# Kernel optimization log

Measured on AMD Instinct MI355X. Metric: run time of the kernel, lower is better.

## Reference

```python
import jax, jax.numpy as jnp
import numpy as np

N_NODES = 100000
N_EDGES = 1600000


def setup_inputs() -> dict:
    key = jax.random.key(0)
    k1, k2, k3, k4 = jax.random.split(key, 4)
    in_c, hid_c, out_c = 128, 128, 64
    x = jax.random.normal(k1, (N_NODES, in_c), dtype=jnp.float32)
    edge_index = jax.random.randint(k2, (2, N_EDGES), 0, N_NODES, dtype=jnp.int64)
    W1 = jax.random.normal(k3, (in_c, hid_c), dtype=jnp.float32) * (1.0 / np.sqrt(in_c))
    b1 = jnp.zeros((hid_c,), dtype=jnp.float32)
    W2 = jax.random.normal(k4, (hid_c, out_c), dtype=jnp.float32) * (1.0 / np.sqrt(hid_c))
    b2 = jnp.zeros((out_c,), dtype=jnp.float32)
    return {"x": x, "edge_index": edge_index, "W1": W1, "b1": b1, "W2": W2, "b2": b2}


def reference(x, edge_index, W1, b1, W2, b2):
    # PyG GCNConv default: add self-loops, symmetric deg normalization, bias.
    N = x.shape[0]
    loops = jnp.arange(N, dtype=edge_index.dtype)
    src = jnp.concatenate([edge_index[0], loops])  # message sources (j)
    dst = jnp.concatenate([edge_index[1], loops])  # aggregation targets (i)
    ones = jnp.ones(src.shape[0], dtype=x.dtype)
    deg = jax.ops.segment_sum(ones, dst, num_segments=N)  # in-degree incl. self-loops
    dis = jnp.where(deg > 0, jax.lax.rsqrt(deg), 0.0)     # deg^{-1/2}, inf->0
    norm = dis[src] * dis[dst]                             # [E+N]

    def gcn(h, W, b):
        h = h @ W                                  # linear transform first (fewer bytes moved)
        msg = h[src] * norm[:, None]               # gather + scale, [E+N, C]
        return jax.ops.segment_sum(msg, dst, num_segments=N) + b

    h = jax.nn.relu(gcn(x, W1, b1))
    return gcn(h, W2, b2)
```

## Files before the change

### kernel.cpp

```cpp
#include <hip/hip_runtime.h>


constexpr int NBKT = 512;
constexpr int EPB  = 4096;
constexpr int CAP  = 8192;

using short8 = __attribute__((ext_vector_type(8))) short;
using f32x4  = __attribute__((ext_vector_type(4))) float;

__device__ __forceinline__ unsigned short f2bf(float f) {
  unsigned u = __float_as_uint(f);
  unsigned r = (u + 0x7FFFu + ((u >> 16) & 1u)) >> 16;
  return (unsigned short)r;
}
__device__ __forceinline__ float bf2f(unsigned short h) {
  return __uint_as_float(((unsigned)h) << 16);
}

__device__ __forceinline__ int ld_idx(const void* ei, int is64, long long i) {
  return is64 ? (int)((const long long*)ei)[i] : ((const int*)ei)[i];
}

__device__ __forceinline__ int sniff64(const unsigned* ei, int tid) {
  unsigned v = (tid < 128) ? ei[2 * tid + 1] : 0u;
  return __syncthreads_or((int)(v != 0u)) ? 0 : 1;
}

__global__ __launch_bounds__(256) void k_partition(const void* __restrict__ ei,
                                                   int* __restrict__ bkt_cursor,
                                                   unsigned* __restrict__ pairbuf,
                                                   int e, int npb) {
  __shared__ int hcnt[NBKT];
  int blk = blockIdx.x, tid = threadIdx.x;
  int is64 = sniff64((const unsigned*)ei, tid);
  for (int i = tid; i < NBKT; i += 256) hcnt[i] = 0;
  __syncthreads();
  int base = blk * EPB;
  int end = base + EPB; if (end > e) end = e;
  for (int i = base + tid; i < end; i += 256) {
    int d = ld_idx(ei, is64, (long long)e + i);
    atomicAdd(&hcnt[d / npb], 1);
  }
  __syncthreads();
  for (int i = tid; i < NBKT; i += 256) {
    int c = hcnt[i];
    hcnt[i] = c ? (i * CAP + atomicAdd(&bkt_cursor[i * 16], c)) : 0;
  }
  __syncthreads();
  for (int i = base + tid; i < end; i += 256) {
    int s = ld_idx(ei, is64, i);
    int d = ld_idx(ei, is64, (long long)e + i);
    int bkt = d / npb;
    int pos = atomicAdd(&hcnt[bkt], 1);
    pairbuf[pos] = (unsigned)s | ((unsigned)(d - bkt * npb) << 20);
  }
}

__global__ __launch_bounds__(256) void k_bucket_all(const unsigned* __restrict__ pairbuf,
                                                    const int* __restrict__ bkt_cursor,
                                                    int2* __restrict__ rowse,
                                                    int* __restrict__ cursor,
                                                    float* __restrict__ dis,
                                                    int* __restrict__ csr,
                                                    int n, int npb) {
  __shared__ int lcsr[CAP];
  __shared__ int cnt[256];
  __shared__ int scn[256];
  int b = blockIdx.x, tid = threadIdx.x;
  int lo = b * npb;
  if (lo >= n) return;
  int hi = lo + npb; if (hi > n) hi = n;
  int nn = hi - lo;
  int seg_base = b * CAP;
  int cnt_total = bkt_cursor[b * 16];

  for (int i = tid; i < nn; i += 256) cnt[i] = 0;
  __syncthreads();
  for (int i = tid; i < cnt_total; i += 256)
    atomicAdd(&cnt[pairbuf[seg_base + i] >> 20], 1);
  __syncthreads();

  int v = (tid < nn) ? cnt[tid] : 0;
  scn[tid] = v;
  __syncthreads();
  for (int off = 1; off < 256; off <<= 1) {
    int t = (tid >= off) ? scn[tid - off] : 0;
    __syncthreads();
    scn[tid] += t;
    __syncthreads();
  }
  int start = (tid == 0) ? 0 : scn[tid - 1];
  if (tid < nn) {
    int node = lo + tid;
    int lo_e = seg_base + start;
    rowse[node] = make_int2(lo_e, lo_e + v);
    cursor[node] = lo_e;
    dis[node] = rsqrtf((float)(v + 1));
  }
  __syncthreads();
  if (tid < nn) cnt[tid] = start;
  __syncthreads();

  if (cnt_total <= CAP) {
    for (int i = tid; i < cnt_total; i += 256) {
      unsigned p = pairbuf[seg_base + i];
      int q = atomicAdd(&cnt[p >> 20], 1);
      lcsr[q] = (int)(p & 0xFFFFFu);
    }
    __syncthreads();
    for (int i = tid; i < cnt_total; i += 256) csr[seg_base + i] = lcsr[i];
  } else {
    for (int i = tid; i < cnt_total; i += 256) {
      unsigned p = pairbuf[seg_base + i];
      int q = atomicAdd(&cursor[lo + (int)(p >> 20)], 1);
      csr[q] = (int)(p & 0xFFFFFu);
    }
  }
}

template <int NCOL, bool XBF16>
__global__ __launch_bounds__(256) void k_gemm_mfma(const void* __restrict__ Xv,
                                                   const float* __restrict__ W,
                                                   const float* __restrict__ dis,
                                                   unsigned short* __restrict__ S,
                                                   int nrows) {
  constexpr int ROWS = 64;
  constexpr int NCF = NCOL / 16;
  __shared__ __align__(16) unsigned short xs[ROWS * 128];
  __shared__ __align__(16) unsigned short wt[NCOL * 128];
  int tid = threadIdx.x;

  for (int id = tid; id < 128 * NCOL; id += 256) {
    int k = id / NCOL, c = id % NCOL;
    wt[(c * 128 + k) ^ ((c & 7) << 3)] = f2bf(W[id]);
  }

  int wv = tid >> 6, lane = tid & 63;
  int l16 = lane & 15, lk = lane >> 4;
  int arow = wv * 16 + l16;
  int npass = (nrows + ROWS - 1) / ROWS;

  for (int p = blockIdx.x; p < npass; p += gridDim.x) {
    int r0 = p * ROWS;
    __syncthreads();
#pragma unroll
    for (int it = 0; it < 4; ++it) {
      int id = tid + 256 * it;
      int row = id >> 4, kc = id & 15;
      int gr = r0 + row;
      unsigned short v[8];
      if (gr < nrows) {
        if (XBF16) {
          const unsigned short* xb = (const unsigned short*)Xv + (size_t)gr * 128 + kc * 8;
#pragma unroll
          for (int j = 0; j < 8; ++j) v[j] = xb[j];
        } else {
          const float4* x4 = (const float4*)Xv + (size_t)gr * 32 + kc * 2;
          float4 f0 = x4[0], f1 = x4[1];
          v[0] = f2bf(f0.x); v[1] = f2bf(f0.y); v[2] = f2bf(f0.z); v[3] = f2bf(f0.w);
          v[4] = f2bf(f1.x); v[5] = f2bf(f1.y); v[6] = f2bf(f1.z); v[7] = f2bf(f1.w);
        }
      } else {
#pragma unroll
        for (int j = 0; j < 8; ++j) v[j] = 0;
      }
      int idx = (row * 128 + kc * 8) ^ ((row & 7) << 3);
      *(short8*)&xs[idx] = *(short8*)v;
    }
    __syncthreads();

    short8 a[4];
#pragma unroll
    for (int ks = 0; ks < 4; ++ks)
      a[ks] = *(short8*)&xs[(arow * 128 + ks * 32 + lk * 8) ^ ((arow & 7) << 3)];

    f32x4 acc[NCF];
#pragma unroll
    for (int cf = 0; cf < NCF; ++cf) acc[cf] = (f32x4){0.f, 0.f, 0.f, 0.f};

#pragma unroll
    for (int cf = 0; cf < NCF; ++cf) {
      int col = cf * 16 + l16;
#pragma unroll
      for (int ks = 0; ks < 4; ++ks) {
        short8 bfr = *(short8*)&wt[(col * 128 + ks * 32 + lk * 8) ^ ((col & 7) << 3)];
        acc[cf] = __builtin_amdgcn_mfma_f32_16x16x32_bf16(a[ks], bfr, acc[cf], 0, 0, 0);
      }
    }

#pragma unroll
    for (int r = 0; r < 4; ++r) {
      int gr = r0 + wv * 16 + lk * 4 + r;
      if (gr < nrows) {
        float dv = dis[gr];
#pragma unroll
        for (int cf = 0; cf < NCF; ++cf)
          S[(size_t)gr * NCOL + cf * 16 + l16] = f2bf(acc[cf][r] * dv);
      }
    }
  }
}

__global__ __launch_bounds__(256) void k_agg1(const unsigned short* __restrict__ S,
                                              const int2* __restrict__ rowse,
                                              const int* __restrict__ csr,
                                              const float* __restrict__ dis,
                                              const float* __restrict__ b1,
                                              unsigned short* __restrict__ H, int n) {
  int node = blockIdx.x * 4 + (threadIdx.x >> 6);
  if (node >= n) return;
  int lane = threadIdx.x & 63;
  int eg = lane >> 4;
  int cp = lane & 15;
  float acc[8];
  if (eg == 0) {
    short8 v = *(const short8*)&S[(size_t)node * 128 + cp * 8];
#pragma unroll
    for (int k = 0; k < 8; ++k) acc[k] = bf2f((unsigned short)v[k]);
  } else {
#pragma unroll
    for (int k = 0; k < 8; ++k) acc[k] = 0.f;
  }
  int2 rp = rowse[node];
  int e = rp.x + eg;
  for (; e + 4 < rp.y; e += 8) {
    int j0 = csr[e], j1 = csr[e + 4];
    short8 v0 = *(const short8*)&S[(size_t)j0 * 128 + cp * 8];
    short8 v1 = *(const short8*)&S[(size_t)j1 * 128 + cp * 8];
#pragma unroll
    for (int k = 0; k < 8; ++k)
      acc[k] += bf2f((unsigned short)v0[k]) + bf2f((unsigned short)v1[k]);
  }
  if (e < rp.y) {
    int j = csr[e];
    short8 v = *(const short8*)&S[(size_t)j * 128 + cp * 8];
#pragma unroll
    for (int k = 0; k < 8; ++k) acc[k] += bf2f((unsigned short)v[k]);
  }
#pragma unroll
  for (int k = 0; k < 8; ++k) {
    acc[k] += __shfl_xor(acc[k], 16);
    acc[k] += __shfl_xor(acc[k], 32);
  }
  if (eg == 0) {
    float d = dis[node];
    float4 bb0 = ((const float4*)b1)[cp * 2];
    float4 bb1 = ((const float4*)b1)[cp * 2 + 1];
    float bv[8] = {bb0.x, bb0.y, bb0.z, bb0.w, bb1.x, bb1.y, bb1.z, bb1.w};
    short8 o;
#pragma unroll
    for (int k = 0; k < 8; ++k)
      o[k] = (short)f2bf(fmaxf(fmaf(acc[k], d, bv[k]), 0.f));
    *(short8*)&H[(size_t)node * 128 + cp * 8] = o;
  }
}

__global__ __launch_bounds__(256) void k_agg2(const unsigned short* __restrict__ S,
                                              const int2* __restrict__ rowse,
                                              const int* __restrict__ csr,
                                              const float* __restrict__ dis,
                                              const float* __restrict__ b2,
                                              float* __restrict__ O, int n) {
  int node = blockIdx.x * 4 + (threadIdx.x >> 6);
  if (node >= n) return;
  int lane = threadIdx.x & 63;
  int eg = lane >> 3;
  int cp = lane & 7;
  float acc[8];
  if (eg == 0) {
    short8 v = *(const short8*)&S[(size_t)node * 64 + cp * 8];
#pragma unroll
    for (int k = 0; k < 8; ++k) acc[k] = bf2f((unsigned short)v[k]);
  } else {
#pragma unroll
    for (int k = 0; k < 8; ++k) acc[k] = 0.f;
  }
  int2 rp = rowse[node];
  int e = rp.x + eg;
  for (; e + 8 < rp.y; e += 16) {
    int j0 = csr[e], j1 = csr[e + 8];
    short8 v0 = *(const short8*)&S[(size_t)j0 * 64 + cp * 8];
    short8 v1 = *(const short8*)&S[(size_t)j1 * 64 + cp * 8];
#pragma unroll
    for (int k = 0; k < 8; ++k)
      acc[k] += bf2f((unsigned short)v0[k]) + bf2f((unsigned short)v1[k]);
  }
  if (e < rp.y) {
    int j = csr[e];
    short8 v = *(const short8*)&S[(size_t)j * 64 + cp * 8];
#pragma unroll
    for (int k = 0; k < 8; ++k) acc[k] += bf2f((unsigned short)v[k]);
  }
#pragma unroll
  for (int k = 0; k < 8; ++k) {
    acc[k] += __shfl_xor(acc[k], 8);
    acc[k] += __shfl_xor(acc[k], 16);
    acc[k] += __shfl_xor(acc[k], 32);
  }
  if (eg == 0) {
    float d = dis[node];
    float4 bb0 = ((const float4*)b2)[cp * 2];
    float4 bb1 = ((const float4*)b2)[cp * 2 + 1];
    float bv[8] = {bb0.x, bb0.y, bb0.z, bb0.w, bb1.x, bb1.y, bb1.z, bb1.w};
    float4 o0, o1;
    o0.x = fmaf(acc[0], d, bv[0]); o0.y = fmaf(acc[1], d, bv[1]);
    o0.z = fmaf(acc[2], d, bv[2]); o0.w = fmaf(acc[3], d, bv[3]);
    o1.x = fmaf(acc[4], d, bv[4]); o1.y = fmaf(acc[5], d, bv[5]);
    o1.z = fmaf(acc[6], d, bv[6]); o1.w = fmaf(acc[7], d, bv[7]);
    ((float4*)O)[(size_t)node * 16 + cp * 2] = o0;
    ((float4*)O)[(size_t)node * 16 + cp * 2 + 1] = o1;
  }
}

extern "C" void kernel_launch(void* const* d_in, const int* in_sizes, int n_in,
                              void* d_out, int out_size, void* d_ws, size_t ws_size,
                              hipStream_t stream) {
  const float* x  = (const float*)d_in[0];
  const void*  ei = d_in[1];
  const float* W1 = (const float*)d_in[2];
  const float* b1 = (const float*)d_in[3];
  const float* W2 = (const float*)d_in[4];
  const float* b2 = (const float*)d_in[5];
  float* out = (float*)d_out;

  const int N = in_sizes[0] / 128;
  const int E = in_sizes[1] / 2;
  const int npb  = (N + NBKT - 1) / NBKT;
  const int nblk = (E + EPB - 1) / EPB;

  char* w = (char*)d_ws;
  size_t off = 0;
  auto alloc = [&](size_t bytes) -> void* {
    void* p = (void*)(w + off);
    off += (bytes + 255) & ~(size_t)255;
    return p;
  };
  int2*           rowse      = (int2*)alloc((size_t)N * 8);
  int*            cursor     = (int*)alloc((size_t)N * 4);
  float*          dis        = (float*)alloc((size_t)N * 4);
  int*            csr        = (int*)alloc((size_t)NBKT * CAP * 4);
  unsigned*       pairbuf    = (unsigned*)alloc((size_t)NBKT * CAP * 4);
  unsigned short* s1         = (unsigned short*)alloc((size_t)N * 128 * 2);
  unsigned short* s2         = (unsigned short*)alloc((size_t)N * 64 * 2);
  unsigned short* h          = (unsigned short*)alloc((size_t)N * 128 * 2);
  int*            bkt_cursor = (int*)alloc((size_t)NBKT * 64);

  hipMemsetAsync(bkt_cursor, 0, (size_t)NBKT * 64, stream);
  k_partition<<<nblk, 256, 0, stream>>>(ei, bkt_cursor, pairbuf, E, npb);
  k_bucket_all<<<NBKT, 256, 0, stream>>>(pairbuf, bkt_cursor, rowse, cursor, dis,
                                         csr, N, npb);

  k_gemm_mfma<128, false><<<1024, 256, 0, stream>>>(x, W1, dis, s1, N);
  k_agg1<<<(N + 3) / 4, 256, 0, stream>>>(s1, rowse, csr, dis, b1, h, N);
  k_gemm_mfma<64, true><<<1024, 256, 0, stream>>>(h, W2, dis, s2, N);
  k_agg2<<<(N + 3) / 4, 256, 0, stream>>>(s2, rowse, csr, dis, b2, out, N);
}
```

Baseline: 200.1 us.

## Fuse first-layer aggregation with second-layer GEMM via MFMA in LDS

Replaces the separate k_agg1 kernel and the second k_gemm_mfma launch with a single kernel, k_agg1_mm. Each 512-thread block aggregates 8 nodes into a bf16 hidden tile in LDS, then runs a 16x16x32 MFMA against W2 to write the scaled s2 rows directly. This removes the global write and re-read of the hidden activation buffer h and one kernel launch. In exchange, every block reloads W2 from global memory and converts it to bf16 in LDS. Half of each MFMA tile is idle because only 8 of its 16 rows hold real nodes.

```diff
diff --git a/kernel.cpp b/kernel.cpp
--- a/kernel.cpp
+++ b/kernel.cpp
@@ -201,57 +201,92 @@
   }
 }
 
-__global__ __launch_bounds__(256) void k_agg1(const unsigned short* __restrict__ S,
-                                              const int2* __restrict__ rowse,
-                                              const int* __restrict__ csr,
-                                              const float* __restrict__ dis,
-                                              const float* __restrict__ b1,
-                                              unsigned short* __restrict__ H, int n) {
-  int node = blockIdx.x * 4 + (threadIdx.x >> 6);
-  if (node >= n) return;
-  int lane = threadIdx.x & 63;
+__global__ __launch_bounds__(512) void k_agg1_mm(const unsigned short* __restrict__ S,
+                                                 const int2* __restrict__ rowse,
+                                                 const int* __restrict__ csr,
+                                                 const float* __restrict__ dis,
+                                                 const float* __restrict__ b1,
+                                                 const float* __restrict__ W2,
+                                                 unsigned short* __restrict__ S2,
+                                                 int n) {
+  __shared__ __align__(16) unsigned short wt2[64 * 128];
+  __shared__ __align__(16) unsigned short hs[16 * 128];
+  int tid = threadIdx.x;
+  for (int id = tid; id < 64 * 128; id += 512) {
+    int k = id >> 6, c = id & 63;
+    wt2[(c * 128 + k) ^ ((c & 7) << 3)] = f2bf(W2[id]);
+  }
+
+  int wv = tid >> 6, lane = tid & 63;
+  int node = blockIdx.x * 8 + wv;
   int eg = lane >> 4;
   int cp = lane & 15;
-  float acc[8];
-  if (eg == 0) {
-    short8 v = *(const short8*)&S[(size_t)node * 128 + cp * 8];
-#pragma unroll
-    for (int k = 0; k < 8; ++k) acc[k] = bf2f((unsigned short)v[k]);
-  } else {
-#pragma unroll
-    for (int k = 0; k < 8; ++k) acc[k] = 0.f;
-  }
-  int2 rp = rowse[node];
-  int e = rp.x + eg;
-  for (; e + 4 < rp.y; e += 8) {
-    int j0 = csr[e], j1 = csr[e + 4];
-    short8 v0 = *(const short8*)&S[(size_t)j0 * 128 + cp * 8];
-    short8 v1 = *(const short8*)&S[(size_t)j1 * 128 + cp * 8];
-#pragma unroll
-    for (int k = 0; k < 8; ++k)
-      acc[k] += bf2f((unsigned short)v0[k]) + bf2f((unsigned short)v1[k]);
-  }
-  if (e < rp.y) {
-    int j = csr[e];
-    short8 v = *(const short8*)&S[(size_t)j * 128 + cp * 8];
-#pragma unroll
-    for (int k = 0; k < 8; ++k) acc[k] += bf2f((unsigned short)v[k]);
-  }
-#pragma unroll
-  for (int k = 0; k < 8; ++k) {
-    acc[k] += __shfl_xor(acc[k], 16);
-    acc[k] += __shfl_xor(acc[k], 32);
-  }
-  if (eg == 0) {
-    float d = dis[node];
-    float4 bb0 = ((const float4*)b1)[cp * 2];
-    float4 bb1 = ((const float4*)b1)[cp * 2 + 1];
-    float bv[8] = {bb0.x, bb0.y, bb0.z, bb0.w, bb1.x, bb1.y, bb1.z, bb1.w};
-    short8 o;
-#pragma unroll
-    for (int k = 0; k < 8; ++k)
-      o[k] = (short)f2bf(fmaxf(fmaf(acc[k], d, bv[k]), 0.f));
-    *(short8*)&H[(size_t)node * 128 + cp * 8] = o;
+
+  if (node < n) {
+    float acc[8];
+    if (eg == 0) {
+      short8 v = *(const short8*)&S[(size_t)node * 128 + cp * 8];
+#pragma unroll
+      for (int k = 0; k < 8; ++k) acc[k] = bf2f((unsigned short)v[k]);
+    } else {
+#pragma unroll
+      for (int k = 0; k < 8; ++k) acc[k] = 0.f;
+    }
+    int2 rp = rowse[node];
+    int e = rp.x + eg;
+    for (; e + 4 < rp.y; e += 8) {
+      int j0 = csr[e], j1 = csr[e + 4];
+      short8 v0 = *(const short8*)&S[(size_t)j0 * 128 + cp * 8];
+      short8 v1 = *(const short8*)&S[(size_t)j1 * 128 + cp * 8];
+#pragma unroll
+      for (int k = 0; k < 8; ++k)
+        acc[k] += bf2f((unsigned short)v0[k]) + bf2f((unsigned short)v1[k]);
+    }
+    if (e < rp.y) {
+      int j = csr[e];
+      short8 v = *(const short8*)&S[(size_t)j * 128 + cp * 8];
+#pragma unroll
+      for (int k = 0; k < 8; ++k) acc[k] += bf2f((unsigned short)v[k]);
+    }
+#pragma unroll
+    for (int k = 0; k < 8; ++k) {
+      acc[k] += __shfl_xor(acc[k], 16);
+      acc[k] += __shfl_xor(acc[k], 32);
+    }
+    if (eg == 0) {
+      float d = dis[node];
+      float4 bb0 = ((const float4*)b1)[cp * 2];
+      float4 bb1 = ((const float4*)b1)[cp * 2 + 1];
+      float bv[8] = {bb0.x, bb0.y, bb0.z, bb0.w, bb1.x, bb1.y, bb1.z, bb1.w};
+      short8 o;
+#pragma unroll
+      for (int k = 0; k < 8; ++k)
+        o[k] = (short)f2bf(fmaxf(fmaf(acc[k], d, bv[k]), 0.f));
+      *(short8*)&hs[(wv * 128 + cp * 8) ^ ((wv & 7) << 3)] = o;
+    }
+  }
+  __syncthreads();
+
+  if (wv < 4) {
+    int l16 = lane & 15, lk = lane >> 4;
+    short8 a[4];
+#pragma unroll
+    for (int ks = 0; ks < 4; ++ks)
+      a[ks] = *(short8*)&hs[(l16 * 128 + ks * 32 + lk * 8) ^ ((l16 & 7) << 3)];
+    f32x4 c_ = (f32x4){0.f, 0.f, 0.f, 0.f};
+    int col = wv * 16 + l16;
+#pragma unroll
+    for (int ks = 0; ks < 4; ++ks) {
+      short8 bfr = *(short8*)&wt2[(col * 128 + ks * 32 + lk * 8) ^ ((col & 7) << 3)];
+      c_ = __builtin_amdgcn_mfma_f32_16x16x32_bf16(a[ks], bfr, c_, 0, 0, 0);
+    }
+#pragma unroll
+    for (int r = 0; r < 4; ++r) {
+      int row = lk * 4 + r;
+      int gr = blockIdx.x * 8 + row;
+      if (row < 8 && gr < n)
+        S2[(size_t)gr * 64 + wv * 16 + l16] = f2bf(c_[r] * dis[gr]);
+    }
   }
 }
 
@@ -342,7 +377,6 @@
   unsigned*       pairbuf    = (unsigned*)alloc((size_t)NBKT * CAP * 4);
   unsigned short* s1         = (unsigned short*)alloc((size_t)N * 128 * 2);
   unsigned short* s2         = (unsigned short*)alloc((size_t)N * 64 * 2);
-  unsigned short* h          = (unsigned short*)alloc((size_t)N * 128 * 2);
   int*            bkt_cursor = (int*)alloc((size_t)NBKT * 64);
 
   hipMemsetAsync(bkt_cursor, 0, (size_t)NBKT * 64, stream);
@@ -351,7 +385,6 @@
                                          csr, N, npb);
 
   k_gemm_mfma<128, false><<<1024, 256, 0, stream>>>(x, W1, dis, s1, N);
-  k_agg1<<<(N + 3) / 4, 256, 0, stream>>>(s1, rowse, csr, dis, b1, h, N);
-  k_gemm_mfma<64, true><<<1024, 256, 0, stream>>>(h, W2, dis, s2, N);
+  k_agg1_mm<<<(N + 7) / 8, 512, 0, stream>>>(s1, rowse, csr, dis, b1, W2, s2, N);
   k_agg2<<<(N + 3) / 4, 256, 0, stream>>>(s2, rowse, csr, dis, b2, out, N);
 }
```

Measured after the change: 217.1 us. 8.5% more time.
